# Performance work log

Hardware: AMD Instinct MI355X
Metric: run time of the kernel (lower is better)

Reference implementation:

```python
import jax, jax.numpy as jnp
import numpy as np

B, T, D, H = 4, 2048, 512, 8
DK = D // H

def setup_inputs() -> dict:
    key = jax.random.key(0)
    ks = jax.random.split(key, 5)
    s = 1.0 / np.sqrt(D)
    return {
        "x": jax.random.normal(ks[0], (B, T, D), dtype=jnp.float32),
        "Wq": jax.random.normal(ks[1], (D, D), dtype=jnp.float32) * s,
        "bq": jnp.zeros((D,), dtype=jnp.float32),
        "Wk": jax.random.normal(ks[2], (D, D), dtype=jnp.float32) * s,
        "bk": jnp.zeros((D,), dtype=jnp.float32),
        "Wv": jax.random.normal(ks[3], (D, D), dtype=jnp.float32) * s,
        "bv": jnp.zeros((D,), dtype=jnp.float32),
        "Wo": jax.random.normal(ks[4], (D, D), dtype=jnp.float32) * s,
        "bo": jnp.zeros((D,), dtype=jnp.float32),
    }

def reference(x, Wq, bq, Wk, bk, Wv, bv, Wo, bo):
    # Linear projections (torch Linear: x @ W.T + b); split into heads.
    q = (x @ Wq.T + bq).reshape(B, T, H, DK)  # [B,T,H,dk]
    k = (x @ Wk.T + bk).reshape(B, T, H, DK)
    v = (x @ Wv.T + bv).reshape(B, T, H, DK)
    scale = 1.0 / np.sqrt(DK)
    # scores: [B,H,T,T]
    scores = jnp.einsum("bqhd,bkhd->bhqk", q, k) * scale
    attn = jax.nn.softmax(scores, axis=-1)
    ctx = jnp.einsum("bhqk,bkhd->bqhd", attn, v).reshape(B, T, D)
    return ctx @ Wo.T + bo
```

## Files before the change

### kernel.cpp

```cpp
#include <hip/hip_runtime.h>
#include <stdint.h>

#define NB 4
#define NT 2048
#define ND 512
#define NH 8
#define NDK 64
#define NM (NB*NT)

typedef __attribute__((ext_vector_type(8))) short short8;
typedef __attribute__((ext_vector_type(4))) float f32x4;

__device__ __forceinline__ unsigned short f2b(float f) {
    union { float f; uint32_t u; } v; v.f = f;
    return (unsigned short)((v.u + 0x7FFFu + ((v.u >> 16) & 1u)) >> 16);
}

__device__ __forceinline__ void load_lds16(const void* g, void* l) {
    void* gn = const_cast<void*>(g);
    __builtin_amdgcn_global_load_lds((__attribute__((address_space(1))) void*)gn,
                                     (__attribute__((address_space(3))) void*)l,
                                     16, 0, 0);
}

__global__ void convert_all(const float* __restrict__ x,  const float* __restrict__ wq,
                            const float* __restrict__ wk, const float* __restrict__ wv,
                            const float* __restrict__ wo, unsigned short* __restrict__ dst) {
    size_t i = ((size_t)blockIdx.x * 256 + threadIdx.x) * 4;
    const float* src; size_t off;
    if (i < 4194304) { src = x; off = i; }
    else {
        size_t j = i - 4194304;
        src = (j < 262144) ? wq : (j < 524288) ? wk : (j < 786432) ? wv : wo;
        off = j & 262143;
    }
    f32x4 v = *(const f32x4*)(src + off);
    ushort4 r;
    r.x = f2b(v[0]); r.y = f2b(v[1]); r.z = f2b(v[2]); r.w = f2b(v[3]);
    *(ushort4*)(dst + i) = r;
}

__global__ __launch_bounds__(256, 3) void proj_gemm(
        const unsigned short* __restrict__ X,
        const unsigned short* __restrict__ Wbase,
        const float* __restrict__ bias0, const float* __restrict__ bias1,
        const float* __restrict__ bias2,
        unsigned short* __restrict__ Obase, unsigned short* __restrict__ VTb,
        float scale0) {
    const int z = blockIdx.z;
    const float* bias = (z == 0) ? bias0 : (z == 1 ? bias1 : bias2);
    const float scale = (z == 0) ? scale0 : 1.0f;

    int rowBase, colBase;
    const unsigned short *Ap, *Bp;
    if (z == 2) {
        rowBase = blockIdx.x * 128;  colBase = blockIdx.y * 128;
        Ap = Wbase + 2 * (ND * ND);  Bp = X;
    } else {
        rowBase = blockIdx.y * 128;  colBase = blockIdx.x * 128;
        Ap = X;                      Bp = Wbase + (size_t)z * (ND * ND);
    }

    __shared__ alignas(16) unsigned short ldsA[128 * 64];
    __shared__ alignas(16) unsigned short ldsW[128 * 64];

    const int tid = threadIdx.x;
    const int lane = tid & 63, wave = tid >> 6;
    const int quad = lane >> 4, l15 = lane & 15;
    const int wm = wave >> 1, wn = wave & 1;

    const int rS = tid >> 3;
    const int gc = (tid & 7) ^ (rS & 7);
    const unsigned short* gA = Ap + (size_t)(rowBase + rS) * ND + gc * 8;
    const unsigned short* gW = Bp + (size_t)(colBase + rS) * ND + gc * 8;
    const int ldst = wave * 512;

    const int swz = l15 & 7;

    f32x4 acc[4][4];
#pragma unroll
    for (int i = 0; i < 4; i++)
#pragma unroll
        for (int j = 0; j < 4; j++) acc[i][j] = (f32x4)0.0f;

    for (int kt = 0; kt < ND / 64; ++kt) {
        __syncthreads();
#pragma unroll
        for (int c = 0; c < 4; ++c) {
            load_lds16(gA + (size_t)c * 32 * ND, ldsA + c * 2048 + ldst);
            load_lds16(gW + (size_t)c * 32 * ND, ldsW + c * 2048 + ldst);
        }
        gA += 64; gW += 64;
        __syncthreads();

#pragma unroll
        for (int ks = 0; ks < 2; ++ks) {
            short8 af[4], bfm[4];
#pragma unroll
            for (int mt = 0; mt < 4; ++mt)
                af[mt] = *(const short8*)(ldsA + (wm * 64 + mt * 16 + l15) * 64
                                          + (((ks * 4 + quad) ^ swz) * 8));
#pragma unroll
            for (int nt = 0; nt < 4; ++nt)
                bfm[nt] = *(const short8*)(ldsW + (wn * 64 + nt * 16 + l15) * 64
                                           + (((ks * 4 + quad) ^ swz) * 8));
#pragma unroll
            for (int mt = 0; mt < 4; ++mt)
#pragma unroll
                for (int nt = 0; nt < 4; ++nt)
                    acc[mt][nt] = __builtin_amdgcn_mfma_f32_16x16x32_bf16(
                        af[mt], bfm[nt], acc[mt][nt], 0, 0, 0);
        }
    }

    if (z == 2) {
        const int bz = colBase >> 11;
        const int t0 = colBase & 2047;
        unsigned short* VTo = VTb + ((size_t)(bz * 512 + rowBase)) * NT + t0;
#pragma unroll
        for (int mt = 0; mt < 4; mt++)
#pragma unroll
            for (int reg = 0; reg < 4; reg++) {
                int m = wm * 64 + mt * 16 + quad * 4 + reg;
                float bm = bias[rowBase + m];
                unsigned short* dst = VTo + (size_t)m * NT + wn * 64 + l15;
#pragma unroll
                for (int nt = 0; nt < 4; nt++)
                    dst[nt * 16] = f2b(acc[mt][nt][reg] + bm);
            }
    } else {
        float biasr[4];
#pragma unroll
        for (int nt = 0; nt < 4; nt++)
            biasr[nt] = bias[colBase + wn * 64 + nt * 16 + l15];
        unsigned short* Oz = Obase + (size_t)z * ((size_t)NM * ND);
#pragma unroll
        for (int mt = 0; mt < 4; mt++) {
            int row = rowBase + wm * 64 + mt * 16 + quad * 4;
#pragma unroll
            for (int reg = 0; reg < 4; reg++) {
                unsigned short* dst = Oz + (size_t)(row + reg) * ND + colBase + wn * 64 + l15;
#pragma unroll
                for (int nt = 0; nt < 4; nt++)
                    dst[nt * 16] = f2b((acc[mt][nt][reg] + biasr[nt]) * scale);
            }
        }
    }
}

__global__ __launch_bounds__(256, 4) void out_gemm(
        const unsigned short* __restrict__ A, const unsigned short* __restrict__ W,
        const float* __restrict__ bias, float* __restrict__ OF) {
    __shared__ alignas(16) unsigned short ldsA[64 * 64];
    __shared__ alignas(16) unsigned short ldsW[128 * 64];

    const int tid = threadIdx.x;
    const int lane = tid & 63, wave = tid >> 6;
    const int quad = lane >> 4, l15 = lane & 15;
    const int wm = wave >> 1, wn = wave & 1;
    const int rowBase = blockIdx.y * 64;
    const int colBase = blockIdx.x * 128;

    const int rS = tid >> 3;
    const int gc = (tid & 7) ^ (rS & 7);
    const unsigned short* gA = A + (size_t)(rowBase + rS) * ND + gc * 8;
    const unsigned short* gW = W + (size_t)(colBase + rS) * ND + gc * 8;
    const int ldst = wave * 512;
    const int swz = l15 & 7;

    f32x4 acc[2][4];
#pragma unroll
    for (int mt = 0; mt < 2; mt++)
#pragma unroll
        for (int nt = 0; nt < 4; nt++) acc[mt][nt] = (f32x4)0.0f;

    for (int kt = 0; kt < ND / 64; ++kt) {
        __syncthreads();
#pragma unroll
        for (int c = 0; c < 2; ++c)
            load_lds16(gA + (size_t)c * 32 * ND, ldsA + c * 2048 + ldst);
#pragma unroll
        for (int c = 0; c < 4; ++c)
            load_lds16(gW + (size_t)c * 32 * ND, ldsW + c * 2048 + ldst);
        gA += 64; gW += 64;
        __syncthreads();

#pragma unroll
        for (int ks = 0; ks < 2; ++ks) {
            short8 af[2], bfm[4];
#pragma unroll
            for (int mt = 0; mt < 2; ++mt)
                af[mt] = *(const short8*)(ldsA + (wm * 32 + mt * 16 + l15) * 64
                                          + (((ks * 4 + quad) ^ swz) * 8));
#pragma unroll
            for (int nt = 0; nt < 4; ++nt)
                bfm[nt] = *(const short8*)(ldsW + (wn * 64 + nt * 16 + l15) * 64
                                           + (((ks * 4 + quad) ^ swz) * 8));
#pragma unroll
            for (int mt = 0; mt < 2; ++mt)
#pragma unroll
                for (int nt = 0; nt < 4; ++nt)
                    acc[mt][nt] = __builtin_amdgcn_mfma_f32_16x16x32_bf16(
                        af[mt], bfm[nt], acc[mt][nt], 0, 0, 0);
        }
    }

    float biasr[4];
#pragma unroll
    for (int nt = 0; nt < 4; nt++)
        biasr[nt] = bias[colBase + wn * 64 + nt * 16 + l15];

#pragma unroll
    for (int mt = 0; mt < 2; mt++)
#pragma unroll
        for (int reg = 0; reg < 4; reg++) {
            int row = rowBase + wm * 32 + mt * 16 + quad * 4 + reg;
            float* dst = OF + (size_t)row * ND + colBase + wn * 64 + l15;
#pragma unroll
            for (int nt = 0; nt < 4; nt++)
                dst[nt * 16] = acc[mt][nt][reg] + biasr[nt];
        }
}

__global__ __launch_bounds__(256, 2) void attn_kernel(
        const unsigned short* __restrict__ Qb, const unsigned short* __restrict__ Kb,
        const unsigned short* __restrict__ VTb, unsigned short* __restrict__ Cb) {
    const int L = blockIdx.x + 16 * (blockIdx.y + 8 * blockIdx.z);
    const int s = L >> 3;
    const int qt = s & 15;
    const int g = (L & 7) + 8 * (s >> 4);
    const int h = g & 7, b = g >> 3;

    __shared__ alignas(16) unsigned short Ks[2 * 8192];
    __shared__ alignas(16) unsigned short Vt[2 * 8192];

    const int tid = threadIdx.x, lane = tid & 63, wave = tid >> 6;
    const int quad = lane >> 4, l15 = lane & 15;
    const size_t headOff = (size_t)h * NDK;
    const size_t rowB = (size_t)b * NT;
    const unsigned short* VT = VTb + (size_t)(b * NH + h) * ((size_t)NDK * NT);

    short8 aq[2][2];
#pragma unroll
    for (int t = 0; t < 2; ++t)
#pragma unroll
        for (int ks = 0; ks < 2; ++ks)
            aq[t][ks] = *(const short8*)(Qb
                + (rowB + qt * 128 + wave * 32 + t * 16 + l15) * ND
                + headOff + ks * 32 + quad * 8);

    const int rK = tid >> 3;
    const int kap = (rK < 16) ? ((rK >> 2) * 8 + (rK & 3))
                              : (((rK - 16) >> 2) * 8 + 4 + ((rK - 16) & 3));
    const int gK8 = (tid & 7) ^ (rK & 7);
    const unsigned short* gK = Kb + (rowB + kap) * ND + headOff + gK8 * 8;
    const int rV = tid >> 4;
    const int gV8 = (tid & 15) ^ (rV & 7);
    const unsigned short* gV = VT + (size_t)rV * NT + gV8 * 8;
    const int ldst = wave * 512;

    const int swz = l15 & 7;
    const int ko0 = l15 * 64 + ((quad ^ swz) * 8);
    const int ko1 = l15 * 64 + (((4 + quad) ^ swz) * 8);

    f32x4 o[2][4];
#pragma unroll
    for (int t = 0; t < 2; ++t)
#pragma unroll
        for (int nt = 0; nt < 4; ++nt) o[t][nt] = (f32x4)0.0f;
    float lacc[2] = {0.0f, 0.0f};

    auto STAGE = [&](int bb, int r) {
        const unsigned short* k = gK + (size_t)r * 128 * ND;
        const unsigned short* v = gV + (size_t)r * 128;
        unsigned short* kd = Ks + bb * 8192 + ldst;
        unsigned short* vd = Vt + bb * 8192 + ldst;
#pragma unroll
        for (int c = 0; c < 4; ++c) {
            load_lds16(k + (size_t)c * 32 * ND, kd + c * 2048);
            load_lds16(v + (size_t)c * 16 * NT, vd + c * 2048);
        }
    };

    STAGE(0, 0);
    __syncthreads();

    for (int kv = 0; kv < 16; ++kv) {
        const int buf = kv & 1;
        if (kv < 15) STAGE(buf ^ 1, kv + 1);

        const unsigned short* KB = Ks + buf * 8192;
        const unsigned short* VB = Vt + buf * 8192;
#pragma unroll
        for (int pb = 0; pb < 4; ++pb) {
            short8 kA0 = *(const short8*)(KB + pb * 2048 + ko0);
            short8 kA1 = *(const short8*)(KB + pb * 2048 + ko1);
            short8 kB0 = *(const short8*)(KB + pb * 2048 + 1024 + ko0);
            short8 kB1 = *(const short8*)(KB + pb * 2048 + 1024 + ko1);
            const int vo = l15 * 128 + (((pb * 4 + quad) ^ swz) * 8);
            short8 vf[4];
#pragma unroll
            for (int nt = 0; nt < 4; ++nt)
                vf[nt] = *(const short8*)(VB + vo + nt * 2048);

#pragma unroll
            for (int t = 0; t < 2; ++t) {
                f32x4 sa = (f32x4)0.0f, sb = (f32x4)0.0f;
                sa = __builtin_amdgcn_mfma_f32_16x16x32_bf16(kA0, aq[t][0], sa, 0, 0, 0);
                sa = __builtin_amdgcn_mfma_f32_16x16x32_bf16(kA1, aq[t][1], sa, 0, 0, 0);
                sb = __builtin_amdgcn_mfma_f32_16x16x32_bf16(kB0, aq[t][0], sb, 0, 0, 0);
                sb = __builtin_amdgcn_mfma_f32_16x16x32_bf16(kB1, aq[t][1], sb, 0, 0, 0);
                float pA0 = exp2f(sa[0]), pA1 = exp2f(sa[1]);
                float pA2 = exp2f(sa[2]), pA3 = exp2f(sa[3]);
                float pB0 = exp2f(sb[0]), pB1 = exp2f(sb[1]);
                float pB2 = exp2f(sb[2]), pB3 = exp2f(sb[3]);
                lacc[t] += ((pA0 + pA1) + (pA2 + pA3)) + ((pB0 + pB1) + (pB2 + pB3));
                union { uint32_t w[4]; short8 v; } cv;
                cv.w[0] = __builtin_amdgcn_perm(__float_as_uint(pA1), __float_as_uint(pA0), 0x07060302u);
                cv.w[1] = __builtin_amdgcn_perm(__float_as_uint(pA3), __float_as_uint(pA2), 0x07060302u);
                cv.w[2] = __builtin_amdgcn_perm(__float_as_uint(pB1), __float_as_uint(pB0), 0x07060302u);
                cv.w[3] = __builtin_amdgcn_perm(__float_as_uint(pB3), __float_as_uint(pB2), 0x07060302u);
#pragma unroll
                for (int nt = 0; nt < 4; ++nt)
                    o[t][nt] = __builtin_amdgcn_mfma_f32_16x16x32_bf16(
                        cv.v, vf[nt], o[t][nt], 0, 0, 0);
            }
        }
        __syncthreads();
    }

#pragma unroll
    for (int t = 0; t < 2; ++t) {
        float la = lacc[t];
        la += __shfl_xor(la, 16);
        la += __shfl_xor(la, 32);
#pragma unroll
        for (int reg = 0; reg < 4; ++reg) {
            float inv = 1.0f / __shfl(la, quad * 4 + reg);
            size_t row = rowB + qt * 128 + wave * 32 + t * 16 + quad * 4 + reg;
#pragma unroll
            for (int nt = 0; nt < 4; ++nt)
                Cb[row * ND + headOff + nt * 16 + l15] = f2b(o[t][nt][reg] * inv);
        }
    }
}

extern "C" void kernel_launch(void* const* d_in, const int* in_sizes, int n_in,
                              void* d_out, int out_size, void* d_ws, size_t ws_size,
                              hipStream_t stream) {
    (void)in_sizes; (void)n_in; (void)out_size; (void)ws_size;
    const float* x  = (const float*)d_in[0];
    const float* Wq = (const float*)d_in[1];
    const float* bq = (const float*)d_in[2];
    const float* Wk = (const float*)d_in[3];
    const float* bk = (const float*)d_in[4];
    const float* Wv = (const float*)d_in[5];
    const float* bv = (const float*)d_in[6];
    const float* Wo = (const float*)d_in[7];
    const float* bo = (const float*)d_in[8];
    float* out = (float*)d_out;

    unsigned short* ws  = (unsigned short*)d_ws;
    unsigned short* xb  = ws;
    unsigned short* wqb = xb + 4194304;
    unsigned short* Qb  = wqb + 4 * 262144;
    unsigned short* Kb  = Qb + 4194304;
    unsigned short* VTb = Kb + 4194304;
    unsigned short* Cb  = VTb + 4194304;
    unsigned short* wob = wqb + 3 * 262144;

    convert_all<<<5120, 256, 0, stream>>>(x, Wq, Wk, Wv, Wo, ws);

    const float qscale = 0.125f * 1.44269504f;
    proj_gemm<<<dim3(4, 64, 3), 256, 0, stream>>>(xb, wqb, bq, bk, bv, Qb, VTb, qscale);
    attn_kernel<<<dim3(16, 8, 4), 256, 0, stream>>>(Qb, Kb, VTb, Cb);
    out_gemm<<<dim3(4, 128), 256, 0, stream>>>(Cb, wob, bo, out);
}
```

Baseline: 172.9 us.

## Split attention KV tile across two wave groups with LDS reduction

Doubles the attention block to 512 threads. Each group of four waves handles half of every 128-key tile, and the two groups' partial output and row-sum accumulators are combined through shared memory at the end. The per-thread staging loads are halved to match. The exp2f calls are also replaced with the raw hardware exp2 builtin. The aim is more waves in flight per CU to hide latency, at the cost of an extra reduction pass and a larger block that may limit occupancy.

```diff
diff --git a/kernel.cpp b/kernel.cpp
--- a/kernel.cpp
+++ b/kernel.cpp
@@ -222,7 +222,7 @@
         }
 }
 
-__global__ __launch_bounds__(256, 2) void attn_kernel(
+__global__ __launch_bounds__(512, 4) void attn_kernel(
         const unsigned short* __restrict__ Qb, const unsigned short* __restrict__ Kb,
         const unsigned short* __restrict__ VTb, unsigned short* __restrict__ Cb) {
     const int L = blockIdx.x + 16 * (blockIdx.y + 8 * blockIdx.z);
@@ -235,6 +235,7 @@
     __shared__ alignas(16) unsigned short Vt[2 * 8192];
 
     const int tid = threadIdx.x, lane = tid & 63, wave = tid >> 6;
+    const int wq = wave & 3, half = wave >> 2;
     const int quad = lane >> 4, l15 = lane & 15;
     const size_t headOff = (size_t)h * NDK;
     const size_t rowB = (size_t)b * NT;
@@ -246,14 +247,15 @@
 #pragma unroll
         for (int ks = 0; ks < 2; ++ks)
             aq[t][ks] = *(const short8*)(Qb
-                + (rowB + qt * 128 + wave * 32 + t * 16 + l15) * ND
+                + (rowB + qt * 128 + wq * 32 + t * 16 + l15) * ND
                 + headOff + ks * 32 + quad * 8);
 
     const int rK = tid >> 3;
-    const int kap = (rK < 16) ? ((rK >> 2) * 8 + (rK & 3))
-                              : (((rK - 16) >> 2) * 8 + 4 + ((rK - 16) & 3));
+    const int rb = rK & 31;
+    const int kap = (rb < 16) ? ((rb >> 2) * 8 + (rb & 3))
+                              : (((rb - 16) >> 2) * 8 + 4 + ((rb - 16) & 3));
     const int gK8 = (tid & 7) ^ (rK & 7);
-    const unsigned short* gK = Kb + (rowB + kap) * ND + headOff + gK8 * 8;
+    const unsigned short* gK = Kb + (rowB + (rK & 32) + kap) * ND + headOff + gK8 * 8;
     const int rV = tid >> 4;
     const int gV8 = (tid & 15) ^ (rV & 7);
     const unsigned short* gV = VT + (size_t)rV * NT + gV8 * 8;
@@ -276,9 +278,9 @@
         unsigned short* kd = Ks + bb * 8192 + ldst;
         unsigned short* vd = Vt + bb * 8192 + ldst;
 #pragma unroll
-        for (int c = 0; c < 4; ++c) {
-            load_lds16(k + (size_t)c * 32 * ND, kd + c * 2048);
-            load_lds16(v + (size_t)c * 16 * NT, vd + c * 2048);
+        for (int c = 0; c < 2; ++c) {
+            load_lds16(k + (size_t)c * 64 * ND, kd + c * 4096);
+            load_lds16(v + (size_t)c * 32 * NT, vd + c * 4096);
         }
     };
 
@@ -292,7 +294,8 @@
         const unsigned short* KB = Ks + buf * 8192;
         const unsigned short* VB = Vt + buf * 8192;
 #pragma unroll
-        for (int pb = 0; pb < 4; ++pb) {
+        for (int pp = 0; pp < 2; ++pp) {
+            const int pb = half * 2 + pp;
             short8 kA0 = *(const short8*)(KB + pb * 2048 + ko0);
             short8 kA1 = *(const short8*)(KB + pb * 2048 + ko1);
             short8 kB0 = *(const short8*)(KB + pb * 2048 + 1024 + ko0);
@@ -310,10 +313,10 @@
                 sa = __builtin_amdgcn_mfma_f32_16x16x32_bf16(kA1, aq[t][1], sa, 0, 0, 0);
                 sb = __builtin_amdgcn_mfma_f32_16x16x32_bf16(kB0, aq[t][0], sb, 0, 0, 0);
                 sb = __builtin_amdgcn_mfma_f32_16x16x32_bf16(kB1, aq[t][1], sb, 0, 0, 0);
-                float pA0 = exp2f(sa[0]), pA1 = exp2f(sa[1]);
-                float pA2 = exp2f(sa[2]), pA3 = exp2f(sa[3]);
-                float pB0 = exp2f(sb[0]), pB1 = exp2f(sb[1]);
-                float pB2 = exp2f(sb[2]), pB3 = exp2f(sb[3]);
+                float pA0 = __builtin_amdgcn_exp2f(sa[0]), pA1 = __builtin_amdgcn_exp2f(sa[1]);
+                float pA2 = __builtin_amdgcn_exp2f(sa[2]), pA3 = __builtin_amdgcn_exp2f(sa[3]);
+                float pB0 = __builtin_amdgcn_exp2f(sb[0]), pB1 = __builtin_amdgcn_exp2f(sb[1]);
+                float pB2 = __builtin_amdgcn_exp2f(sb[2]), pB3 = __builtin_amdgcn_exp2f(sb[3]);
                 lacc[t] += ((pA0 + pA1) + (pA2 + pA3)) + ((pB0 + pB1) + (pB2 + pB3));
                 union { uint32_t w[4]; short8 v; } cv;
                 cv.w[0] = __builtin_amdgcn_perm(__float_as_uint(pA1), __float_as_uint(pA0), 0x07060302u);
@@ -329,18 +332,35 @@
         __syncthreads();
     }
 
-#pragma unroll
-    for (int t = 0; t < 2; ++t) {
-        float la = lacc[t];
-        la += __shfl_xor(la, 16);
-        la += __shfl_xor(la, 32);
-#pragma unroll
-        for (int reg = 0; reg < 4; ++reg) {
-            float inv = 1.0f / __shfl(la, quad * 4 + reg);
-            size_t row = rowB + qt * 128 + wave * 32 + t * 16 + quad * 4 + reg;
-#pragma unroll
-            for (int nt = 0; nt < 4; ++nt)
-                Cb[row * ND + headOff + nt * 16 + l15] = f2b(o[t][nt][reg] * inv);
+    f32x4* sc4 = (f32x4*)Ks;
+    float* scl = (float*)Vt;
+    if (half) {
+#pragma unroll
+        for (int t = 0; t < 2; ++t) {
+            scl[(wq * 64 + lane) * 2 + t] = lacc[t];
+#pragma unroll
+            for (int nt = 0; nt < 4; ++nt)
+                sc4[((wq * 64 + lane) * 2 + t) * 4 + nt] = o[t][nt];
+        }
+    }
+    __syncthreads();
+    if (!half) {
+#pragma unroll
+        for (int t = 0; t < 2; ++t) {
+            float la = lacc[t] + scl[(wq * 64 + lane) * 2 + t];
+            la += __shfl_xor(la, 16);
+            la += __shfl_xor(la, 32);
+#pragma unroll
+            for (int nt = 0; nt < 4; ++nt)
+                o[t][nt] += sc4[((wq * 64 + lane) * 2 + t) * 4 + nt];
+#pragma unroll
+            for (int reg = 0; reg < 4; ++reg) {
+                float inv = 1.0f / __shfl(la, quad * 4 + reg);
+                size_t row = rowB + qt * 128 + wq * 32 + t * 16 + quad * 4 + reg;
+#pragma unroll
+                for (int nt = 0; nt < 4; ++nt)
+                    Cb[row * ND + headOff + nt * 16 + l15] = f2b(o[t][nt][reg] * inv);
+            }
         }
     }
 }
@@ -373,6 +393,6 @@
 
     const float qscale = 0.125f * 1.44269504f;
     proj_gemm<<<dim3(4, 64, 3), 256, 0, stream>>>(xb, wqb, bq, bk, bv, Qb, VTb, qscale);
-    attn_kernel<<<dim3(16, 8, 4), 256, 0, stream>>>(Qb, Kb, VTb, Cb);
+    attn_kernel<<<dim3(16, 8, 4), 512, 0, stream>>>(Qb, Kb, VTb, Cb);
     out_gemm<<<dim3(4, 128), 256, 0, stream>>>(Cb, wob, bo, out);
 }
```

Result: faster. 167.8 us (-2.9%).
